# Optimization experiments

Hardware: AMD Instinct MI355X
Metric: run time of the kernel (lower is better)

Reference implementation:

```python
import jax, jax.numpy as jnp
import numpy as np


def setup_inputs() -> dict:
    key = jax.random.key(0)
    k0, k1, k2, k3, k4 = jax.random.split(key, 5)
    K, LENGTH, D, B, MAXDEPTH = 50000, 65536, 128, 1024, 16
    weights = jax.random.normal(k0, (LENGTH, D), dtype=jnp.float32)
    x = jax.random.normal(k1, (B, D), dtype=jnp.float32)
    y = jax.random.randint(k2, (B,), 0, K, dtype=jnp.int64)
    # padded per-class paths of internal (pseudo-class) nodes; real paths index [K, LENGTH)
    path_idx = jax.random.randint(k3, (K, MAXDEPTH), 0, LENGTH, dtype=jnp.int64)
    path_len = jax.random.randint(k4, (K,), 0, MAXDEPTH, dtype=jnp.int32)
    return {"weights": weights, "x": x, "y": y, "path_idx": path_idx, "path_len": path_len}


def reference(weights, x, y, path_idx, path_len):
    # weights: [LENGTH, d]; x: [B, d]; y: [B]; path_idx: [K, Dmax]; path_len: [K]
    K, Dmax = path_idx.shape
    # mask out padded path slots (original loops over len(path)-1 real ancestors)
    mask = (jnp.arange(Dmax)[None, :] < path_len[:, None]).astype(weights.dtype)  # [K, Dmax]
    # gather ancestor rows and sum along the path; add the class's own row j
    path_sum = jnp.einsum("kpd,kp->kd", weights[path_idx], mask)  # [K, d]
    added_weights = weights[:K] + path_sum                        # [K, d]
    logits = x @ added_weights.T                                  # [B, K]
    logp = jax.nn.log_softmax(logits, axis=-1)
    loss = -jnp.take_along_axis(logp, y[:, None], axis=1).mean()  # CrossEntropyLoss (mean)
    return loss, logits, added_weights
```

## Files before the change

### kernel.cpp

```cpp
#include <hip/hip_runtime.h>
#include <math.h>

#define KCLS  50000
#define KP    50048
#define DIM   128
#define BATCH 1024
#define MAXD  16

#define NBLK_N   (KP / 128)
#define NSG      ((NBLK_N + 7) / 8)
#define GEMM_GRID (NSG * 64)
#define NBP      (NBLK_N * 2)
#define CLS_BLOCKS (KP / 8)
#define XB_BLOCKS  (BATCH * DIM / 1024)

typedef __attribute__((ext_vector_type(8))) short short8;
typedef __attribute__((ext_vector_type(4))) float floatx4;

__device__ __forceinline__ unsigned short f2bf(float f) {
    unsigned u = __float_as_uint(f);
    u += 0x7fffu + ((u >> 16) & 1u);
    return (unsigned short)(u >> 16);
}

__global__ __launch_bounds__(256) void aw_kernel(
    const float* __restrict__ weights, const int* __restrict__ path_idx,
    const int* __restrict__ path_len, float* __restrict__ aw,
    unsigned short* __restrict__ awb,
    const float* __restrict__ x, unsigned short* __restrict__ xb,
    float* __restrict__ loss)
{
    int t = threadIdx.x;

    if (blockIdx.x >= CLS_BLOCKS) {
        if (blockIdx.x == CLS_BLOCKS && t == 0) *loss = 0.f;
        int i = ((blockIdx.x - CLS_BLOCKS) * 256 + t) * 4;
        float4 v = *(const float4*)(x + i);
        ushort4 hv = { f2bf(v.x), f2bf(v.y), f2bf(v.z), f2bf(v.w) };
        *(ushort4*)(xb + i) = hv;
        return;
    }

    int wv_id = t >> 6;
    int lane  = t & 63;
    int half  = lane >> 5;
    int li    = lane & 31;
    int k     = blockIdx.x * 8 + wv_id * 2 + half;
    int col   = li * 4;

    bool valid = k < KCLS;
    int kc = valid ? k : 0;

    float4 acc = {0.f, 0.f, 0.f, 0.f};
    int plen = 0;
    if (valid) {
        acc  = *(const float4*)(weights + (size_t)k * DIM + col);
        plen = path_len[k];
    }
    const int* pp = path_idx + (size_t)kc * MAXD;

    {
        int idx[8];
        #pragma unroll
        for (int p = 0; p < 8; ++p) idx[p] = pp[p];
        float4 wvv[8];
        #pragma unroll
        for (int p = 0; p < 8; ++p)
            wvv[p] = *(const float4*)(weights + (size_t)idx[p] * DIM + col);
        #pragma unroll
        for (int p = 0; p < 8; ++p) {
            float m = (p < plen) ? 1.f : 0.f;
            acc.x += m * wvv[p].x; acc.y += m * wvv[p].y;
            acc.z += m * wvv[p].z; acc.w += m * wvv[p].w;
        }
    }
    if (__any(plen > 8)) {
        int idx[8];
        #pragma unroll
        for (int p = 0; p < 8; ++p) idx[p] = pp[8 + p];
        float4 wvv[8];
        #pragma unroll
        for (int p = 0; p < 8; ++p)
            wvv[p] = *(const float4*)(weights + (size_t)idx[p] * DIM + col);
        #pragma unroll
        for (int p = 0; p < 8; ++p) {
            float m = (8 + p < plen) ? 1.f : 0.f;
            acc.x += m * wvv[p].x; acc.y += m * wvv[p].y;
            acc.z += m * wvv[p].z; acc.w += m * wvv[p].w;
        }
    }

    if (valid)
        *(float4*)(aw + (size_t)k * DIM + col) = acc;
    ushort4 hv = { f2bf(acc.x), f2bf(acc.y), f2bf(acc.z), f2bf(acc.w) };
    *(ushort4*)(awb + (size_t)k * DIM + col) = hv;
}

template<bool PART>
__global__ __launch_bounds__(256) void gemm_kernel(
    const unsigned short* __restrict__ Xb,
    const unsigned short* __restrict__ Wb,
    float* __restrict__ logits,
    float2* __restrict__ part)
{
    int id = blockIdx.x;
    int sg = id >> 6, bx = (id & 63) >> 3, c = id & 7;
    int by = sg * 8 + c;
    if (by >= NBLK_N) return;

    int tid = threadIdx.x;
    int wave = tid >> 6, lane = tid & 63;
    int r = lane & 15, quad = lane >> 4;
    int m0 = bx * 128 + (wave >> 1) * 64;
    int n0 = by * 128 + (wave & 1) * 64;

    const unsigned short* wp = Wb + (size_t)(n0 + r) * DIM + quad * 8;
    const unsigned short* xp = Xb + (size_t)(m0 + r) * DIM + quad * 8;

    floatx4 acc[4][4];
    #pragma unroll
    for (int i = 0; i < 4; ++i)
        #pragma unroll
        for (int j = 0; j < 4; ++j)
            acc[i][j] = (floatx4){0.f, 0.f, 0.f, 0.f};

    #pragma unroll
    for (int kk = 0; kk < 4; ++kk) {
        short8 a[4], b[4];
        #pragma unroll
        for (int i = 0; i < 4; ++i)
            a[i] = *(const short8*)(wp + (size_t)(i * 16) * DIM + kk * 32);
        #pragma unroll
        for (int j = 0; j < 4; ++j)
            b[j] = *(const short8*)(xp + (size_t)(j * 16) * DIM + kk * 32);
        #pragma unroll
        for (int i = 0; i < 4; ++i)
            #pragma unroll
            for (int j = 0; j < 4; ++j)
                acc[i][j] = __builtin_amdgcn_mfma_f32_16x16x32_bf16(
                    a[i], b[j], acc[i][j], 0, 0, 0);
    }

    #pragma unroll
    for (int j = 0; j < 4; ++j) {
        int mrow = m0 + j * 16 + r;
        float* rowp = logits + (size_t)mrow * KCLS;

        #pragma unroll
        for (int i = 0; i < 4; ++i) {
            int nb = n0 + i * 16 + quad * 4;
            if (nb < KCLS)
                *(floatx4*)(rowp + nb) = acc[i][j];
        }

        if constexpr (PART) {
            float mx = -INFINITY;
            #pragma unroll
            for (int i = 0; i < 4; ++i) {
                bool ok = (n0 + i * 16 + quad * 4) < KCLS;
                #pragma unroll
                for (int reg = 0; reg < 4; ++reg) {
                    float v = ok ? acc[i][j][reg] : -INFINITY;
                    mx = fmaxf(mx, v);
                }
            }
            mx = fmaxf(mx, __shfl_xor(mx, 16));
            mx = fmaxf(mx, __shfl_xor(mx, 32));
            float s = 0.f;
            #pragma unroll
            for (int i = 0; i < 4; ++i) {
                bool ok = (n0 + i * 16 + quad * 4) < KCLS;
                #pragma unroll
                for (int reg = 0; reg < 4; ++reg) {
                    float v = ok ? acc[i][j][reg] : -INFINITY;
                    s += __expf(v - mx);
                }
            }
            s += __shfl_xor(s, 16);
            s += __shfl_xor(s, 32);
            if (quad == 0)
                part[(size_t)mrow * NBP + by * 2 + (wave & 1)]
                    = make_float2(mx, s);
        }
    }
}

__global__ __launch_bounds__(256) void lsereduce_kernel(
    const float2* __restrict__ part, const float* __restrict__ logits,
    const int* __restrict__ y, float* __restrict__ loss)
{
    int b = blockIdx.x * 4 + (threadIdx.x >> 6);
    int lane = threadIdx.x & 63;
    const float2* pr = part + (size_t)b * NBP;

    float m = -INFINITY, s = 0.f;
    for (int i = lane; i < NBP; i += 64) {
        float2 pv = pr[i];
        if (pv.x > m) {
            s = s * __expf(m - pv.x) + pv.y;
            m = pv.x;
        } else {
            s += pv.y * __expf(pv.x - m);
        }
    }
    #pragma unroll
    for (int off = 32; off; off >>= 1) {
        float m2 = __shfl_xor(m, off);
        float s2 = __shfl_xor(s, off);
        float M = fmaxf(m, m2);
        s = s * __expf(m - M) + s2 * __expf(m2 - M);
        m = M;
    }
    if (lane == 0) {
        float lse = m + __logf(s);
        float ly = logits[(size_t)b * KCLS + y[b]];
        atomicAdd(loss, (lse - ly) * (1.0f / BATCH));
    }
}

__global__ __launch_bounds__(256) void lse_kernel(
    const float* __restrict__ logits, const int* __restrict__ y,
    float* __restrict__ loss)
{
    int b = blockIdx.x;
    const float* row = logits + (size_t)b * KCLS;
    float m = -INFINITY, s = 0.f;

    auto upd = [&](float v) {
        if (v <= m) {
            s += __expf(v - m);
        } else {
            s = s * __expf(m - v) + 1.f;
            m = v;
        }
    };

    if (threadIdx.x < 3) upd(row[threadIdx.x]);
    const float4* rv = (const float4*)(row + 3);
    for (int i = threadIdx.x; i < 12499; i += 256) {
        float4 v = rv[i];
        upd(v.x); upd(v.y); upd(v.z); upd(v.w);
    }
    if (threadIdx.x == 3) upd(row[49999]);

    #pragma unroll
    for (int off = 32; off > 0; off >>= 1) {
        float m2 = __shfl_down(m, off);
        float s2 = __shfl_down(s, off);
        float M = fmaxf(m, m2);
        s = s * __expf(m - M) + s2 * __expf(m2 - M);
        m = M;
    }
    __shared__ float sm[4], ss[4];
    int w = threadIdx.x >> 6, l = threadIdx.x & 63;
    if (l == 0) { sm[w] = m; ss[w] = s; }
    __syncthreads();
    if (threadIdx.x == 0) {
        m = sm[0]; s = ss[0];
        #pragma unroll
        for (int i = 1; i < 4; ++i) {
            float M = fmaxf(m, sm[i]);
            s = s * __expf(m - M) + ss[i] * __expf(sm[i] - M);
            m = M;
        }
        float lse = m + __logf(s);
        float ly = row[y[b]];
        atomicAdd(loss, (lse - ly) * (1.0f / BATCH));
    }
}

extern "C" void kernel_launch(void* const* d_in, const int* in_sizes, int n_in,
                              void* d_out, int out_size, void* d_ws, size_t ws_size,
                              hipStream_t stream)
{
    const float* weights  = (const float*)d_in[0];
    const float* x        = (const float*)d_in[1];
    const int*   y        = (const int*)d_in[2];
    const int*   path_idx = (const int*)d_in[3];
    const int*   path_len = (const int*)d_in[4];

    float* out    = (float*)d_out;
    float* loss   = out;
    float* logits = out + 1;
    float* aw     = out + 1 + (size_t)BATCH * KCLS;

    size_t awb_sz  = (size_t)KP * DIM * sizeof(unsigned short);
    size_t xb_sz   = (size_t)BATCH * DIM * sizeof(unsigned short);
    size_t part_sz = (size_t)BATCH * NBP * sizeof(float2);

    unsigned short* awb = (unsigned short*)d_ws;
    unsigned short* xb  = awb + (size_t)KP * DIM;
    float2* part = (float2*)((char*)d_ws + awb_sz + xb_sz);
    bool fused = ws_size >= awb_sz + xb_sz + part_sz;


    aw_kernel<<<CLS_BLOCKS + XB_BLOCKS, 256, 0, stream>>>(
        weights, path_idx, path_len, aw, awb, x, xb, loss);

    if (fused) {
        gemm_kernel<true><<<GEMM_GRID, 256, 0, stream>>>(
            xb, awb, logits, part);
        lsereduce_kernel<<<BATCH / 4, 256, 0, stream>>>(part, logits, y, loss);
    } else {
        gemm_kernel<false><<<GEMM_GRID, 256, 0, stream>>>(
            xb, awb, logits, nullptr);
        lse_kernel<<<BATCH, 256, 0, stream>>>(logits, y, loss);
    }
}
```

Measured before the change: 391.2 us.

## Software-pipeline added-weights build with GEMM chunks across staged launches

Merges the added-weights gather kernel and the bf16 GEMM into one kernel template whose blocks act either as GEMM tiles or as gather blocks. The host then issues five staged launches, each running the GEMM for class chunk i alongside the gather for chunk i+1, so the memory-bound gather overlaps with the MFMA work. This trades the loss of the grouped tile-swizzle raster and extra launch overhead for overlap between the two phases.

After: 402.9 us. +3.0%, slower.

```diff
diff --git a/kernel.cpp b/kernel.cpp
--- a/kernel.cpp
+++ b/kernel.cpp
@@ -7,12 +7,9 @@
 #define BATCH 1024
 #define MAXD  16
 
-#define NBLK_N   (KP / 128)
-#define NSG      ((NBLK_N + 7) / 8)
-#define GEMM_GRID (NSG * 64)
+#define NBLK_N   391
 #define NBP      (NBLK_N * 2)
-#define CLS_BLOCKS (KP / 8)
-#define XB_BLOCKS  (BATCH * DIM / 1024)
+#define XB_BLOCKS 128
 
 typedef __attribute__((ext_vector_type(8))) short short8;
 typedef __attribute__((ext_vector_type(4))) float floatx4;
@@ -23,166 +20,163 @@
     return (unsigned short)(u >> 16);
 }
 
-__global__ __launch_bounds__(256) void aw_kernel(
+template<bool PART>
+__global__ __launch_bounds__(256) void fused_kernel(
     const float* __restrict__ weights, const int* __restrict__ path_idx,
     const int* __restrict__ path_len, float* __restrict__ aw,
     unsigned short* __restrict__ awb,
     const float* __restrict__ x, unsigned short* __restrict__ xb,
-    float* __restrict__ loss)
+    float* __restrict__ logits, float2* __restrict__ part,
+    float* __restrict__ loss,
+    int gemm_cb0, int ngemm, int aw_cls0, int aw_nblk)
 {
+    int bid = blockIdx.x;
     int t = threadIdx.x;
 
-    if (blockIdx.x >= CLS_BLOCKS) {
-        if (blockIdx.x == CLS_BLOCKS && t == 0) *loss = 0.f;
-        int i = ((blockIdx.x - CLS_BLOCKS) * 256 + t) * 4;
-        float4 v = *(const float4*)(x + i);
-        ushort4 hv = { f2bf(v.x), f2bf(v.y), f2bf(v.z), f2bf(v.w) };
-        *(ushort4*)(xb + i) = hv;
-        return;
-    }
-
-    int wv_id = t >> 6;
-    int lane  = t & 63;
-    int half  = lane >> 5;
-    int li    = lane & 31;
-    int k     = blockIdx.x * 8 + wv_id * 2 + half;
-    int col   = li * 4;
-
-    bool valid = k < KCLS;
-    int kc = valid ? k : 0;
-
-    float4 acc = {0.f, 0.f, 0.f, 0.f};
-    int plen = 0;
-    if (valid) {
-        acc  = *(const float4*)(weights + (size_t)k * DIM + col);
-        plen = path_len[k];
-    }
-    const int* pp = path_idx + (size_t)kc * MAXD;
-
-    {
-        int idx[8];
-        #pragma unroll
-        for (int p = 0; p < 8; ++p) idx[p] = pp[p];
-        float4 wvv[8];
-        #pragma unroll
-        for (int p = 0; p < 8; ++p)
-            wvv[p] = *(const float4*)(weights + (size_t)idx[p] * DIM + col);
-        #pragma unroll
-        for (int p = 0; p < 8; ++p) {
-            float m = (p < plen) ? 1.f : 0.f;
-            acc.x += m * wvv[p].x; acc.y += m * wvv[p].y;
-            acc.z += m * wvv[p].z; acc.w += m * wvv[p].w;
-        }
-    }
-    if (__any(plen > 8)) {
-        int idx[8];
-        #pragma unroll
-        for (int p = 0; p < 8; ++p) idx[p] = pp[8 + p];
-        float4 wvv[8];
-        #pragma unroll
-        for (int p = 0; p < 8; ++p)
-            wvv[p] = *(const float4*)(weights + (size_t)idx[p] * DIM + col);
-        #pragma unroll
-        for (int p = 0; p < 8; ++p) {
-            float m = (8 + p < plen) ? 1.f : 0.f;
-            acc.x += m * wvv[p].x; acc.y += m * wvv[p].y;
-            acc.z += m * wvv[p].z; acc.w += m * wvv[p].w;
-        }
-    }
-
-    if (valid)
-        *(float4*)(aw + (size_t)k * DIM + col) = acc;
-    ushort4 hv = { f2bf(acc.x), f2bf(acc.y), f2bf(acc.z), f2bf(acc.w) };
-    *(ushort4*)(awb + (size_t)k * DIM + col) = hv;
-}
-
-template<bool PART>
-__global__ __launch_bounds__(256) void gemm_kernel(
-    const unsigned short* __restrict__ Xb,
-    const unsigned short* __restrict__ Wb,
-    float* __restrict__ logits,
-    float2* __restrict__ part)
-{
-    int id = blockIdx.x;
-    int sg = id >> 6, bx = (id & 63) >> 3, c = id & 7;
-    int by = sg * 8 + c;
-    if (by >= NBLK_N) return;
-
-    int tid = threadIdx.x;
-    int wave = tid >> 6, lane = tid & 63;
-    int r = lane & 15, quad = lane >> 4;
-    int m0 = bx * 128 + (wave >> 1) * 64;
-    int n0 = by * 128 + (wave & 1) * 64;
-
-    const unsigned short* wp = Wb + (size_t)(n0 + r) * DIM + quad * 8;
-    const unsigned short* xp = Xb + (size_t)(m0 + r) * DIM + quad * 8;
-
-    floatx4 acc[4][4];
-    #pragma unroll
-    for (int i = 0; i < 4; ++i)
-        #pragma unroll
-        for (int j = 0; j < 4; ++j)
-            acc[i][j] = (floatx4){0.f, 0.f, 0.f, 0.f};
-
-    #pragma unroll
-    for (int kk = 0; kk < 4; ++kk) {
-        short8 a[4], b[4];
+    if (bid < ngemm) {
+        int bx = bid & 7;
+        int by = gemm_cb0 + (bid >> 3);
+        int wave = t >> 6, lane = t & 63;
+        int r = lane & 15, quad = lane >> 4;
+        int m0 = bx * 128 + (wave >> 1) * 64;
+        int n0 = by * 128 + (wave & 1) * 64;
+
+        const unsigned short* wp = awb + (size_t)(n0 + r) * DIM + quad * 8;
+        const unsigned short* xp = xb  + (size_t)(m0 + r) * DIM + quad * 8;
+
+        floatx4 acc[4][4];
         #pragma unroll
         for (int i = 0; i < 4; ++i)
-            a[i] = *(const short8*)(wp + (size_t)(i * 16) * DIM + kk * 32);
+            #pragma unroll
+            for (int j = 0; j < 4; ++j)
+                acc[i][j] = (floatx4){0.f, 0.f, 0.f, 0.f};
+
         #pragma unroll
-        for (int j = 0; j < 4; ++j)
-            b[j] = *(const short8*)(xp + (size_t)(j * 16) * DIM + kk * 32);
+        for (int kk = 0; kk < 4; ++kk) {
+            short8 a[4], b[4];
+            #pragma unroll
+            for (int i = 0; i < 4; ++i)
+                a[i] = *(const short8*)(wp + (size_t)(i * 16) * DIM + kk * 32);
+            #pragma unroll
+            for (int j = 0; j < 4; ++j)
+                b[j] = *(const short8*)(xp + (size_t)(j * 16) * DIM + kk * 32);
+            #pragma unroll
+            for (int i = 0; i < 4; ++i)
+                #pragma unroll
+                for (int j = 0; j < 4; ++j)
+                    acc[i][j] = __builtin_amdgcn_mfma_f32_16x16x32_bf16(
+                        a[i], b[j], acc[i][j], 0, 0, 0);
+        }
+
         #pragma unroll
-        for (int i = 0; i < 4; ++i)
-            #pragma unroll
-            for (int j = 0; j < 4; ++j)
-                acc[i][j] = __builtin_amdgcn_mfma_f32_16x16x32_bf16(
-                    a[i], b[j], acc[i][j], 0, 0, 0);
-    }
-
-    #pragma unroll
-    for (int j = 0; j < 4; ++j) {
-        int mrow = m0 + j * 16 + r;
-        float* rowp = logits + (size_t)mrow * KCLS;
-
-        #pragma unroll
-        for (int i = 0; i < 4; ++i) {
-            int nb = n0 + i * 16 + quad * 4;
-            if (nb < KCLS)
-                *(floatx4*)(rowp + nb) = acc[i][j];
-        }
-
-        if constexpr (PART) {
-            float mx = -INFINITY;
+        for (int j = 0; j < 4; ++j) {
+            int mrow = m0 + j * 16 + r;
+            float* rowp = logits + (size_t)mrow * KCLS;
+
             #pragma unroll
             for (int i = 0; i < 4; ++i) {
-                bool ok = (n0 + i * 16 + quad * 4) < KCLS;
+                int nb = n0 + i * 16 + quad * 4;
+                if (nb < KCLS)
+                    *(floatx4*)(rowp + nb) = acc[i][j];
+            }
+
+            if constexpr (PART) {
+                float mx = -INFINITY;
                 #pragma unroll
-                for (int reg = 0; reg < 4; ++reg) {
-                    float v = ok ? acc[i][j][reg] : -INFINITY;
-                    mx = fmaxf(mx, v);
+                for (int i = 0; i < 4; ++i) {
+                    bool ok = (n0 + i * 16 + quad * 4) < KCLS;
+                    #pragma unroll
+                    for (int reg = 0; reg < 4; ++reg) {
+                        float v = ok ? acc[i][j][reg] : -INFINITY;
+                        mx = fmaxf(mx, v);
+                    }
                 }
+                mx = fmaxf(mx, __shfl_xor(mx, 16));
+                mx = fmaxf(mx, __shfl_xor(mx, 32));
+                float s = 0.f;
+                #pragma unroll
+                for (int i = 0; i < 4; ++i) {
+                    bool ok = (n0 + i * 16 + quad * 4) < KCLS;
+                    #pragma unroll
+                    for (int reg = 0; reg < 4; ++reg) {
+                        float v = ok ? acc[i][j][reg] : -INFINITY;
+                        s += __expf(v - mx);
+                    }
+                }
+                s += __shfl_xor(s, 16);
+                s += __shfl_xor(s, 32);
+                if (quad == 0)
+                    part[(size_t)mrow * NBP + by * 2 + (wave & 1)]
+                        = make_float2(mx, s);
             }
-            mx = fmaxf(mx, __shfl_xor(mx, 16));
-            mx = fmaxf(mx, __shfl_xor(mx, 32));
-            float s = 0.f;
-            #pragma unroll
-            for (int i = 0; i < 4; ++i) {
-                bool ok = (n0 + i * 16 + quad * 4) < KCLS;
-                #pragma unroll
-                for (int reg = 0; reg < 4; ++reg) {
-                    float v = ok ? acc[i][j][reg] : -INFINITY;
-                    s += __expf(v - mx);
-                }
+        }
+        return;
+    }
+
+    int abid = bid - ngemm;
+    if (abid < aw_nblk) {
+        int wv_id = t >> 6;
+        int lane  = t & 63;
+        int half  = lane >> 5;
+        int li    = lane & 31;
+        int k     = aw_cls0 + abid * 8 + wv_id * 2 + half;
+        int col   = li * 4;
+
+        bool valid = k < KCLS;
+        int kc = valid ? k : 0;
+
+        float4 acc = {0.f, 0.f, 0.f, 0.f};
+        int plen = 0;
+        if (valid) {
+            acc  = *(const float4*)(weights + (size_t)k * DIM + col);
+            plen = path_len[k];
+        }
+        const int* pp = path_idx + (size_t)kc * MAXD;
+
+        {
+            int idx[8];
+            #pragma unroll
+            for (int p = 0; p < 8; ++p) idx[p] = pp[p];
+            float4 wvv[8];
+            #pragma unroll
+            for (int p = 0; p < 8; ++p)
+                wvv[p] = *(const float4*)(weights + (size_t)idx[p] * DIM + col);
+            #pragma unroll
+            for (int p = 0; p < 8; ++p) {
+                float m = (p < plen) ? 1.f : 0.f;
+                acc.x += m * wvv[p].x; acc.y += m * wvv[p].y;
+                acc.z += m * wvv[p].z; acc.w += m * wvv[p].w;
             }
-            s += __shfl_xor(s, 16);
-            s += __shfl_xor(s, 32);
-            if (quad == 0)
-                part[(size_t)mrow * NBP + by * 2 + (wave & 1)]
-                    = make_float2(mx, s);
-        }
-    }
+        }
+        if (__any(plen > 8)) {
+            int idx[8];
+            #pragma unroll
+            for (int p = 0; p < 8; ++p) idx[p] = pp[8 + p];
+            float4 wvv[8];
+            #pragma unroll
+            for (int p = 0; p < 8; ++p)
+                wvv[p] = *(const float4*)(weights + (size_t)idx[p] * DIM + col);
+            #pragma unroll
+            for (int p = 0; p < 8; ++p) {
+                float m = (8 + p < plen) ? 1.f : 0.f;
+                acc.x += m * wvv[p].x; acc.y += m * wvv[p].y;
+                acc.z += m * wvv[p].z; acc.w += m * wvv[p].w;
+            }
+        }
+
+        if (valid)
+            *(float4*)(aw + (size_t)k * DIM + col) = acc;
+        ushort4 hv = { f2bf(acc.x), f2bf(acc.y), f2bf(acc.z), f2bf(acc.w) };
+        *(ushort4*)(awb + (size_t)k * DIM + col) = hv;
+        return;
+    }
+
+    int xi = abid - aw_nblk;
+    if (xi == 0 && t == 0) *loss = 0.f;
+    int i = (xi * 256 + t) * 4;
+    float4 v = *(const float4*)(x + i);
+    ushort4 hv = { f2bf(v.x), f2bf(v.y), f2bf(v.z), f2bf(v.w) };
+    *(ushort4*)(xb + i) = hv;
 }
 
 __global__ __launch_bounds__(256) void lsereduce_kernel(
@@ -293,17 +287,30 @@
     float2* part = (float2*)((char*)d_ws + awb_sz + xb_sz);
     bool fused = ws_size >= awb_sz + xb_sz + part_sz;
 
-
-    aw_kernel<<<CLS_BLOCKS + XB_BLOCKS, 256, 0, stream>>>(
-        weights, path_idx, path_len, aw, awb, x, xb, loss);
-
     if (fused) {
-        gemm_kernel<true><<<GEMM_GRID, 256, 0, stream>>>(
-            xb, awb, logits, part);
+        fused_kernel<true><<<1568 + XB_BLOCKS, 256, 0, stream>>>(
+            weights, path_idx, path_len, aw, awb, x, xb, logits, part, loss,
+            0, 0, 0, 1568);
+        fused_kernel<true><<<98 * 8 + 1568, 256, 0, stream>>>(
+            weights, path_idx, path_len, aw, awb, x, xb, logits, part, loss,
+            0, 98 * 8, 12544, 1568);
+        fused_kernel<true><<<98 * 8 + 1568, 256, 0, stream>>>(
+            weights, path_idx, path_len, aw, awb, x, xb, logits, part, loss,
+            98, 98 * 8, 25088, 1568);
+        fused_kernel<true><<<98 * 8 + 1552, 256, 0, stream>>>(
+            weights, path_idx, path_len, aw, awb, x, xb, logits, part, loss,
+            196, 98 * 8, 37632, 1552);
+        fused_kernel<true><<<97 * 8, 256, 0, stream>>>(
+            weights, path_idx, path_len, aw, awb, x, xb, logits, part, loss,
+            294, 97 * 8, 0, 0);
         lsereduce_kernel<<<BATCH / 4, 256, 0, stream>>>(part, logits, y, loss);
     } else {
-        gemm_kernel<false><<<GEMM_GRID, 256, 0, stream>>>(
-            xb, awb, logits, nullptr);
+        fused_kernel<false><<<6256 + XB_BLOCKS, 256, 0, stream>>>(
+            weights, path_idx, path_len, aw, awb, x, xb, logits, nullptr, loss,
+            0, 0, 0, 6256);
+        fused_kernel<false><<<NBLK_N * 8, 256, 0, stream>>>(
+            weights, path_idx, path_len, aw, awb, x, xb, logits, nullptr, loss,
+            0, NBLK_N * 8, 0, 0);
         lse_kernel<<<BATCH, 256, 0, stream>>>(logits, y, loss);
     }
 }
```
